# Kernel tuning notes

Measured on AMD Instinct MI355X. Metric: run time of the kernel, lower is better.

The kernel has to match this reference:

```python
import jax, jax.numpy as jnp
import numpy as np
import math

B, S, F, H, C = 64, 64, 4096, 1024, 31


def setup_inputs() -> dict:
    key = jax.random.key(0)
    ks = jax.random.split(key, 10)
    inp = {
        "x": jax.random.normal(ks[0], (B, S, F), dtype=jnp.float32),
        "h0": jax.random.normal(ks[1], (B, H), dtype=jnp.float32),
        "Wxe": jax.random.normal(ks[2], (F, H), dtype=jnp.float32) / math.sqrt(F),
        "bxe": jnp.zeros((H,), jnp.float32),
        "Wep": jax.random.normal(ks[3], (H, C), dtype=jnp.float32) / math.sqrt(H),
        "bep": jnp.zeros((C,), jnp.float32),
        "Whr": jax.random.normal(ks[4], (H, H), dtype=jnp.float32) / math.sqrt(H),
        "bhr": jnp.zeros((H,), jnp.float32),
        "Wx0r": jax.random.normal(ks[5], (H, H), dtype=jnp.float32) / math.sqrt(H),
        "bx0r": jnp.zeros((H,), jnp.float32),
        "Wxtz": jax.random.normal(ks[6], (H, H), dtype=jnp.float32) / math.sqrt(H),
        "bxtz": jnp.zeros((H,), jnp.float32),
        "Wx0z": jax.random.normal(ks[7], (H, H), dtype=jnp.float32) / math.sqrt(H),
        "bx0z": jnp.zeros((H,), jnp.float32),
        "Wxth1": jax.random.normal(ks[8], (H, H), dtype=jnp.float32) / math.sqrt(H),
        "bxth1": jnp.zeros((H,), jnp.float32),
        "Wh1h1": jax.random.normal(ks[9], (H, H), dtype=jnp.float32) / math.sqrt(H),
        "bh1h1": jnp.zeros((H,), jnp.float32),
    }
    return inp


def reference(x, h0, Wxe, bxe, Wep, bep, Whr, bhr, Wx0r, bx0r,
              Wxtz, bxtz, Wx0z, bx0z, Wxth1, bxth1, Wh1h1, bh1h1):
    # x: (B, S, F); h0: (B, H)
    steps = x.shape[1]
    x0 = x[:, -1]                                            # current information

    # Input-dependent projections are independent of the recurrence -> batch them.
    xtes = jax.nn.relu(jnp.einsum('bsf,fh->bsh', x, Wxe) + bxe)   # (B,S,H)
    x0e = jax.nn.relu(x0 @ Wxe + bxe)                             # (B,H), constant over steps
    ptes = jnp.einsum('bsh,hc->bsc', xtes, Wep) + bep             # (B,S,C)
    p0e = x0e @ Wep + bep                                         # (B,C)

    x0r = x0e @ Wx0r + bx0r                                       # (B,H) step-invariant
    x0z = x0e @ Wx0z + bx0z
    xtz_all = jnp.einsum('bsh,hg->bsg', xtes, Wxtz) + bxtz        # (B,S,H)
    xth1_all = jnp.einsum('bsh,hg->bsg', xtes, Wxth1) + bxth1     # (B,S,H)

    def step(h, inputs):
        xtz, xth1 = inputs                                        # (B,H) each
        rt = jax.nn.sigmoid(h @ Whr + bhr + x0r)
        zt = jax.nn.sigmoid(xtz + x0z)
        h1_t_1 = h @ Wh1h1 + bh1h1
        ht1 = jnp.tanh(xth1 + rt * h1_t_1)
        ht = (1.0 - zt) * ht1 + zt * h
        return ht, ht

    # scan over time: move step axis to front
    xs = (jnp.swapaxes(xtz_all, 0, 1), jnp.swapaxes(xth1_all, 0, 1))  # (S,B,H)
    _, hts_t = jax.lax.scan(step, h0, xs)
    hts = jnp.swapaxes(hts_t, 0, 1)                               # (B,S,H)

    p0es = jnp.broadcast_to(p0e[:, None, :], (p0e.shape[0], steps, p0e.shape[1]))
    x0es = jnp.broadcast_to(x0e[:, None, :], (x0e.shape[0], steps, x0e.shape[1]))
    return (hts, ptes, p0es, x0es * 1.0, xtes) if False else (hts, ptes, p0es, xtes, x0es)
```

## Files before the change

### kernel.cpp

```cpp
#include <hip/hip_runtime.h>
#include <stdint.h>


using bf16 = __bf16;
typedef __attribute__((ext_vector_type(8))) __bf16 bf16x8;
typedef __attribute__((ext_vector_type(4))) float f32x4;

#define B_DIM 64
#define S_DIM 64
#define F_DIM 4096
#define H_DIM 1024
#define C_DIM 31

__global__ void cast_tag_kernel(const float* __restrict__ x, bf16* __restrict__ xbf,
                                const float* __restrict__ h0, unsigned* __restrict__ hT0) {
  int bx = blockIdx.x;
  if (bx < 8192) {
    int i = bx * 256 + threadIdx.x;
    const float4* p = (const float4*)x + (size_t)i * 2;
    float4 a = p[0], b = p[1];
    bf16x8 v;
    v[0] = (bf16)a.x; v[1] = (bf16)a.y; v[2] = (bf16)a.z; v[3] = (bf16)a.w;
    v[4] = (bf16)b.x; v[5] = (bf16)b.y; v[6] = (bf16)b.z; v[7] = (bf16)b.w;
    ((bf16x8*)xbf)[i] = v;
  } else {
    int i = (bx - 8192) * 256 + threadIdx.x;
    union { bf16 b; unsigned short u; } cv;
    cv.b = (bf16)h0[i];
    __hip_atomic_store(hT0 + i, ((unsigned)cv.u << 16), __ATOMIC_RELAXED,
                       __HIP_MEMORY_SCOPE_AGENT);
  }
}

__device__ __forceinline__ void tr64(const float* __restrict__ in, bf16* __restrict__ out,
                                     int R, int C, int tR, int tC) {
  __shared__ float t[64][65];
  int tx = threadIdx.x & 63, ty = threadIdx.x >> 6;
#pragma unroll
  for (int i = 0; i < 16; ++i) {
    int r = tR + i * 4 + ty, c = tC + tx;
    t[i * 4 + ty][tx] = (r < R && c < C) ? in[(size_t)r * C + c] : 0.f;
  }
  __syncthreads();
#pragma unroll
  for (int i = 0; i < 16; ++i) {
    int c = tC + i * 4 + ty, r = tR + tx;
    if (c < C && r < R) out[(size_t)c * R + r] = (bf16)t[tx][i * 4 + ty];
  }
}

__global__ void transpose_all(const float* __restrict__ Wxe, bf16* __restrict__ WxeT,
                              const float* __restrict__ a0, const float* __restrict__ a1,
                              const float* __restrict__ a2, const float* __restrict__ a3,
                              const float* __restrict__ a4, const float* __restrict__ a5,
                              bf16* __restrict__ o0, bf16* __restrict__ o1,
                              bf16* __restrict__ o2,
                              const float* __restrict__ Wep, bf16* __restrict__ WepT) {
  int id = blockIdx.x;
  if (id < 1024) {
    tr64(Wxe, WxeT, 4096, 1024, (id & 63) * 64, (id >> 6) * 64);
  } else if (id < 2560) {
    int q = id - 1024, z = q >> 8, t = q & 255;
    const float* in = z == 0 ? a0 : z == 1 ? a1 : z == 2 ? a2 : z == 3 ? a3 : z == 4 ? a4 : a5;
    bf16* out = (z < 2 ? o0 : z < 4 ? o1 : o2) + (size_t)(z & 1) * 1048576;
    tr64(in, out, 1024, 1024, (t & 15) * 64, (t >> 4) * 64);
  } else {
    tr64(Wep, WepT, 1024, 31, (id - 2560) * 64, 0);
  }
}

__global__ void bcast_x0es(const float* __restrict__ xtesO, float* __restrict__ x0es) {
  int b = blockIdx.x >> 4, c = blockIdx.x & 15;
  float4 v = ((const float4*)(xtesO + ((size_t)b * 64 + 63) * 1024))[threadIdx.x];
  float4* dst = (float4*)(x0es + (size_t)b * 65536 + (size_t)c * 4096) + threadIdx.x;
#pragma unroll
  for (int i = 0; i < 4; ++i) dst[i * 256] = v;
}

template <int MODE>
__launch_bounds__(256, 2)
__global__ void gemm_bt(const bf16* __restrict__ A, const bf16* __restrict__ B,
                        int M, int N, int K, int lda,
                        const float* __restrict__ bias0,
                        const float* __restrict__ bias1,
                        const float* __restrict__ bias2,
                        const float* __restrict__ x0rz,
                        float* __restrict__ outA,
                        float* __restrict__ outB,
                        float* __restrict__ outC,
                        float* __restrict__ outD,
                        bf16* __restrict__ outBf) {
  __shared__ bf16 ldsA[128 * 64];
  __shared__ bf16 ldsB[128 * 64];
  const int tid = threadIdx.x;
  const int lane = tid & 63;
  const int wave = tid >> 6;
  const int quad = lane >> 4;
  const int l15 = lane & 15;
  const int wm = wave & 1, wn = wave >> 1;
  const int m0 = blockIdx.x * 128, n0 = blockIdx.y * 128;
  const int kPer = K / gridDim.z;
  const int k0 = blockIdx.z * kPer;

  f32x4 acc[4][4] = {};

  for (int kc = k0; kc < k0 + kPer; kc += 64) {
#pragma unroll
    for (int i = 0; i < 4; ++i) {
      int qb = i * 256 + wave * 64;
      int q = qb + lane;
      int r = q >> 3, cs = q & 7;
      int c = cs ^ (r & 7);
      int gr = m0 + r; if (gr > M - 1) gr = M - 1;
      __builtin_amdgcn_global_load_lds(
          (const __attribute__((address_space(1))) unsigned int*)(A + (size_t)gr * lda + kc + c * 8),
          (__attribute__((address_space(3))) unsigned int*)(ldsA + (size_t)qb * 8),
          16, 0, 0);
      __builtin_amdgcn_global_load_lds(
          (const __attribute__((address_space(1))) unsigned int*)(B + (size_t)(n0 + r) * K + kc + c * 8),
          (__attribute__((address_space(3))) unsigned int*)(ldsB + (size_t)qb * 8),
          16, 0, 0);
    }
    __syncthreads();
#pragma unroll
    for (int ks = 0; ks < 2; ++ks) {
      bf16x8 af[4], bfr[4];
      int ch = ks * 4 + quad;
#pragma unroll
      for (int t = 0; t < 4; ++t) {
        int ar = wm * 64 + t * 16 + l15;
        af[t] = *(const bf16x8*)(ldsA + ar * 64 + ((ch ^ (ar & 7)) * 8));
        int br = wn * 64 + t * 16 + l15;
        bfr[t] = *(const bf16x8*)(ldsB + br * 64 + ((ch ^ (br & 7)) * 8));
      }
#pragma unroll
      for (int mt = 0; mt < 4; ++mt)
#pragma unroll
        for (int nt = 0; nt < 4; ++nt)
          acc[mt][nt] = __builtin_amdgcn_mfma_f32_16x16x32_bf16(
              af[mt], bfr[nt], acc[mt][nt], 0, 0, 0);
    }
    __syncthreads();
  }

#pragma unroll
  for (int mt = 0; mt < 4; ++mt) {
#pragma unroll
    for (int nt = 0; nt < 4; ++nt) {
#pragma unroll
      for (int i = 0; i < 4; ++i) {
        int m = m0 + wm * 64 + mt * 16 + quad * 4 + i;
        int n = n0 + wn * 64 + nt * 16 + l15;
        if (m >= M) continue;
        float v = acc[mt][nt][i];
        if (MODE == 0) {
          v += bias0[n];
          v = fmaxf(v, 0.f);
          outA[(size_t)m * 1024 + n] = v;
          outBf[(size_t)m * 1024 + n] = (bf16)v;
        } else if (MODE == 1) {
          if (n < 1024) {
            float z = v + bias0[n] + x0rz[(size_t)(m >> 6) * 2048 + 1024 + n];
            outA[(size_t)m * 1024 + n] =
                __builtin_amdgcn_rcpf(1.f + __expf(-z));
          } else if (n < 2048) {
            outB[(size_t)m * 1024 + (n - 1024)] = v + bias1[n - 1024];
          } else if (n < 2048 + C_DIM) {
            float pv = v + bias2[n - 2048];
            outC[(size_t)m * C_DIM + (n - 2048)] = pv;
            if ((m & 63) == 63) {
              size_t base = (size_t)(m >> 6) * 64 * C_DIM + (n - 2048);
              for (int sp = 0; sp < 64; ++sp) outD[base + (size_t)sp * C_DIM] = pv;
            }
          }
        } else {
          if (k0 == 0) v += (n < 1024 ? bias0[n] : bias1[n - 1024]);
          atomicAdd(outA + (size_t)m * 2048 + n, v);
        }
      }
    }
  }
}

#define TAG_OK(v, w) \
  ((((unsigned)(v) & 0xFFFFu) == (w)) & (((unsigned)((v) >> 32) & 0xFFFFu) == (w)))

__launch_bounds__(256, 1)
__global__ void recur_kernel(const bf16* __restrict__ WrecT,
                             const float* __restrict__ bhr,
                             const float* __restrict__ bh1h1,
                             const float* __restrict__ x0rz,
                             const float* __restrict__ ztAll,
                             const float* __restrict__ xth1All,
                             const float* __restrict__ h0,
                             unsigned* hT0,
                             unsigned* hT1,
                             float* __restrict__ hts) {
  __shared__ bf16 ldsA[2][16 * 1024];
  const int tid = threadIdx.x;
  const int lane = tid & 63, wave = tid >> 6;
  const int quad = lane >> 4, l15 = lane & 15;
  const int j = blockIdx.x >> 2;
  const int g = blockIdx.x & 3;
  const int col = j * 64 + wave * 16 + l15;

  bf16x8 wr[32], wh[32];
#pragma unroll
  for (int kb = 0; kb < 32; ++kb) {
    wr[kb] = *(const bf16x8*)(WrecT + (size_t)col * 1024 + kb * 32 + quad * 8);
    wh[kb] = *(const bf16x8*)(WrecT + (size_t)(1024 + col) * 1024 + kb * 32 + quad * 8);
  }
  float hb_ = bh1h1[col];
  float rb[4], hloc[4];
#pragma unroll
  for (int i = 0; i < 4; ++i) {
    int b = g * 16 + quad * 4 + i;
    rb[i] = bhr[col] + x0rz[(size_t)b * 2048 + col];
    hloc[i] = h0[(size_t)b * 1024 + col];
  }

  const int off0 = ((quad ^ (l15 & 7)) * 16);
  const int off1 = (((4 + quad) ^ (l15 & 7)) * 16);

  for (int s = 0; s < 64; ++s) {
    const unsigned want = (unsigned)s;
    const unsigned long long* __restrict__ src =
        (const unsigned long long*)(((s & 1) ? hT1 : hT0) + (size_t)g * 16384) + tid * 2;

    unsigned long long qa[16], qb[16];
#pragma unroll
    for (int r = 0; r < 16; ++r) {
      qa[r] = __hip_atomic_load(src + (size_t)r * 512, __ATOMIC_RELAXED,
                                __HIP_MEMORY_SCOPE_AGENT);
      qb[r] = __hip_atomic_load(src + (size_t)r * 512 + 1, __ATOMIC_RELAXED,
                                __HIP_MEMORY_SCOPE_AGENT);
    }
    float zt[4], xh[4];
#pragma unroll
    for (int i = 0; i < 4; ++i) {
      size_t mrow = ((size_t)(g * 16 + quad * 4 + i) * 64 + s) * 1024 + col;
      zt[i] = ztAll[mrow];
      xh[i] = xth1All[mrow];
    }
    for (int it = 0; ; ++it) {
      unsigned miss = 0;
#pragma unroll
      for (int r = 0; r < 16; ++r)
        if (!(TAG_OK(qa[r], want) & TAG_OK(qb[r], want))) miss |= 1u << r;
      if (!miss || it > (1 << 17)) break;
#pragma unroll
      for (int r = 0; r < 16; ++r) {
        qa[r] = __hip_atomic_load(src + (size_t)r * 512, __ATOMIC_RELAXED,
                                  __HIP_MEMORY_SCOPE_AGENT);
        qb[r] = __hip_atomic_load(src + (size_t)r * 512 + 1, __ATOMIC_RELAXED,
                                  __HIP_MEMORY_SCOPE_AGENT);
      }
    }
    bf16* dstL = ldsA[s & 1];
#pragma unroll
    for (int r = 0; r < 16; ++r) {
      unsigned d0 = (unsigned)qa[r], d1 = (unsigned)(qa[r] >> 32);
      unsigned d2 = (unsigned)qb[r], d3 = (unsigned)(qb[r] >> 32);
      unsigned long long pk =
          ((unsigned long long)((d2 >> 16) | (d3 & 0xFFFF0000u)) << 32) |
          ((d0 >> 16) | (d1 & 0xFFFF0000u));
      int cc = ((tid >> 1) & 0x78) | (((tid >> 1) ^ r) & 7);
      *(unsigned long long*)((char*)dstL + r * 2048 + cc * 16 + (tid & 1) * 8) = pk;
    }
    __syncthreads();

    f32x4 racc0 = {0.f, 0.f, 0.f, 0.f}, racc1 = {0.f, 0.f, 0.f, 0.f};
    f32x4 hacc0 = {0.f, 0.f, 0.f, 0.f}, hacc1 = {0.f, 0.f, 0.f, 0.f};
    const char* baseL = (const char*)dstL + l15 * 2048;
#pragma unroll
    for (int kb = 0; kb < 32; kb += 2) {
      bf16x8 af0 = *(const bf16x8*)(baseL + (kb >> 1) * 128 + off0);
      bf16x8 af1 = *(const bf16x8*)(baseL + (kb >> 1) * 128 + off1);
      racc0 = __builtin_amdgcn_mfma_f32_16x16x32_bf16(af0, wr[kb], racc0, 0, 0, 0);
      hacc0 = __builtin_amdgcn_mfma_f32_16x16x32_bf16(af0, wh[kb], hacc0, 0, 0, 0);
      racc1 = __builtin_amdgcn_mfma_f32_16x16x32_bf16(af1, wr[kb + 1], racc1, 0, 0, 0);
      hacc1 = __builtin_amdgcn_mfma_f32_16x16x32_bf16(af1, wh[kb + 1], hacc1, 0, 0, 0);
    }

    unsigned* dst = (s & 1) ? hT0 : hT1;
    float hn[4];
#pragma unroll
    for (int i = 0; i < 4; ++i) {
      float ra = racc0[i] + racc1[i];
      float ha = hacc0[i] + hacc1[i];
      float rt = __builtin_amdgcn_rcpf(1.f + __expf(-(ra + rb[i])));
      float e2 = __expf(2.f * (xh[i] + rt * (ha + hb_)));
      float th = 1.f - 2.f * __builtin_amdgcn_rcpf(e2 + 1.f);
      hn[i] = (1.f - zt[i]) * th + zt[i] * hloc[i];
      hloc[i] = hn[i];
    }
    if (s < 63) {
#pragma unroll
      for (int i = 0; i < 4; ++i) {
        int b = g * 16 + quad * 4 + i;
        union { bf16 b16; unsigned short u; } cv;
        cv.b16 = (bf16)hn[i];
        __hip_atomic_store(dst + (size_t)b * 1024 + col,
                           ((unsigned)cv.u << 16) | (unsigned)(s + 1),
                           __ATOMIC_RELAXED, __HIP_MEMORY_SCOPE_AGENT);
      }
    }
#pragma unroll
    for (int i = 0; i < 4; ++i) {
      size_t mrow = ((size_t)(g * 16 + quad * 4 + i) * 64 + s) * 1024 + col;
      hts[mrow] = hn[i];
    }
  }
}

extern "C" void kernel_launch(void* const* d_in, const int* in_sizes, int n_in,
                              void* d_out, int out_size, void* d_ws, size_t ws_size,
                              hipStream_t stream) {
  const float* x     = (const float*)d_in[0];
  const float* h0    = (const float*)d_in[1];
  const float* Wxe   = (const float*)d_in[2];
  const float* bxe   = (const float*)d_in[3];
  const float* Wep   = (const float*)d_in[4];
  const float* bep   = (const float*)d_in[5];
  const float* Whr   = (const float*)d_in[6];
  const float* bhr   = (const float*)d_in[7];
  const float* Wx0r  = (const float*)d_in[8];
  const float* bx0r  = (const float*)d_in[9];
  const float* Wxtz  = (const float*)d_in[10];
  const float* bxtz  = (const float*)d_in[11];
  const float* Wx0z  = (const float*)d_in[12];
  const float* bx0z  = (const float*)d_in[13];
  const float* Wxth1 = (const float*)d_in[14];
  const float* bxth1 = (const float*)d_in[15];
  const float* Wh1h1 = (const float*)d_in[16];
  const float* bh1h1 = (const float*)d_in[17];

  float* out   = (float*)d_out;
  float* hts   = out;
  float* ptes  = out + 4194304;
  float* p0es  = out + 4321280;
  float* xtesO = out + 4448256;
  float* x0es  = out + 8642560;

  char* ws = (char*)d_ws;
  size_t off = 0;
  auto alloc = [&](size_t bytes) -> char* {
    char* p = ws + off;
    off += (bytes + 255) & ~(size_t)255;
    return p;
  };
  bf16*  xbf     = (bf16*)alloc(33554432);
  float* ztAll   = (float*)xbf;
  float* xth1All = (float*)((char*)xbf + 16777216);
  bf16*  WxeT    = (bf16*)alloc(8388608);
  bf16*  W2T     = (bf16*)alloc((size_t)2176 * 1024 * 2);
  bf16*  WrecT   = (bf16*)alloc(4194304);
  bf16*  Wx0T    = (bf16*)alloc(4194304);
  bf16*  xtesBf  = (bf16*)alloc(8388608);
  float* x0rz    = (float*)alloc(524288);
  unsigned* hT0  = (unsigned*)alloc(262144);
  unsigned* hT1  = (unsigned*)alloc(262144);

  hipMemsetAsync(W2T, 0, (size_t)2176 * 1024 * 2, stream);
  hipMemsetAsync(x0rz, 0, 524288, stream);

  dim3 tb(256);
  cast_tag_kernel<<<8448, tb, 0, stream>>>(x, xbf, h0, hT0);
  transpose_all<<<2576, tb, 0, stream>>>(Wxe, WxeT,
                                         Whr, Wh1h1, Wxtz, Wxth1, Wx0r, Wx0z,
                                         WrecT, W2T, Wx0T,
                                         Wep, W2T + 2048 * 1024);

  gemm_bt<0><<<dim3(32, 8), tb, 0, stream>>>(xbf, WxeT, 4096, 1024, 4096, 4096,
                                             bxe, nullptr, nullptr, nullptr,
                                             xtesO, nullptr, nullptr, nullptr, xtesBf);
  bcast_x0es<<<1024, tb, 0, stream>>>(xtesO, x0es);
  gemm_bt<2><<<dim3(1, 16, 4), tb, 0, stream>>>(xtesBf + 63 * 1024, Wx0T, 64, 2048, 1024, 65536,
                                                bx0r, bx0z, nullptr, nullptr,
                                                x0rz, nullptr, nullptr, nullptr, nullptr);
  gemm_bt<1><<<dim3(32, 17), tb, 0, stream>>>(xtesBf, W2T, 4096, 2176, 1024, 1024,
                                              bxtz, bxth1, bep, x0rz,
                                              ztAll, xth1All, ptes, p0es, nullptr);

  recur_kernel<<<64, tb, 0, stream>>>(WrecT, bhr, bh1h1, x0rz, ztAll, xth1All,
                                      h0, hT0, hT1, hts);
}
```

Before: 634.8 us.

## Split recurrence into 8 batch groups and add per-wave step flags for sync

The recurrent kernel now runs on 128 blocks, each handling 8 batch rows instead of 16. Only half the MFMA rows are used, and half of each wave's lanes sit idle in the elementwise part. Cross-block synchronisation moves from polling every tagged h value to polling a compact array of per-wave step flags. The h data is prefetched with sc0 loads before the flag spin, and the tag check is kept as a fallback. The goal is to shorten the serial per-step latency by spreading the step over more CUs and polling less data, at the cost of wasted MFMA work and a more complex memory-ordering protocol.

```diff
diff --git a/kernel.cpp b/kernel.cpp
--- a/kernel.cpp
+++ b/kernel.cpp
@@ -185,6 +185,16 @@
 #define TAG_OK(v, w) \
   ((((unsigned)(v) & 0xFFFFu) == (w)) & (((unsigned)((v) >> 32) & 0xFFFFu) == (w)))
 
+__device__ __forceinline__ unsigned long long sc0_load_u64(const unsigned long long* p) {
+  unsigned long long v;
+  asm volatile("global_load_dwordx2 %0, %1, off sc0" : "=v"(v) : "v"(p));
+  return v;
+}
+__device__ __forceinline__ void wait_vm0() {
+  asm volatile("s_waitcnt vmcnt(0)" ::: "memory");
+  __builtin_amdgcn_sched_barrier(0);
+}
+
 __launch_bounds__(256, 1)
 __global__ void recur_kernel(const bf16* __restrict__ WrecT,
                              const float* __restrict__ bhr,
@@ -195,13 +205,14 @@
                              const float* __restrict__ h0,
                              unsigned* hT0,
                              unsigned* hT1,
+                             unsigned* flags,
                              float* __restrict__ hts) {
-  __shared__ bf16 ldsA[2][16 * 1024];
+  __shared__ bf16 ldsA[2][8 * 1024];
   const int tid = threadIdx.x;
   const int lane = tid & 63, wave = tid >> 6;
   const int quad = lane >> 4, l15 = lane & 15;
-  const int j = blockIdx.x >> 2;
-  const int g = blockIdx.x & 3;
+  const int j = blockIdx.x >> 3;
+  const int g = blockIdx.x & 7;
   const int col = j * 64 + wave * 16 + l15;
 
   bf16x8 wr[32], wh[32];
@@ -211,54 +222,99 @@
     wh[kb] = *(const bf16x8*)(WrecT + (size_t)(1024 + col) * 1024 + kb * 32 + quad * 8);
   }
   float hb_ = bh1h1[col];
-  float rb[4], hloc[4];
-#pragma unroll
-  for (int i = 0; i < 4; ++i) {
-    int b = g * 16 + quad * 4 + i;
-    rb[i] = bhr[col] + x0rz[(size_t)b * 2048 + col];
-    hloc[i] = h0[(size_t)b * 1024 + col];
+  float rb[4] = {}, hloc[4] = {};
+  if (quad < 2) {
+#pragma unroll
+    for (int i = 0; i < 4; ++i) {
+      int b = g * 8 + quad * 4 + i;
+      rb[i] = bhr[col] + x0rz[(size_t)b * 2048 + col];
+      hloc[i] = h0[(size_t)b * 1024 + col];
+    }
   }
 
   const int off0 = ((quad ^ (l15 & 7)) * 16);
   const int off1 = (((4 + quad) ^ (l15 & 7)) * 16);
+
+  unsigned* fl = flags + g * 64;
+  const int myflag = j * 4 + wave;
 
   for (int s = 0; s < 64; ++s) {
     const unsigned want = (unsigned)s;
     const unsigned long long* __restrict__ src =
-        (const unsigned long long*)(((s & 1) ? hT1 : hT0) + (size_t)g * 16384) + tid * 2;
-
-    unsigned long long qa[16], qb[16];
-#pragma unroll
-    for (int r = 0; r < 16; ++r) {
-      qa[r] = __hip_atomic_load(src + (size_t)r * 512, __ATOMIC_RELAXED,
-                                __HIP_MEMORY_SCOPE_AGENT);
-      qb[r] = __hip_atomic_load(src + (size_t)r * 512 + 1, __ATOMIC_RELAXED,
-                                __HIP_MEMORY_SCOPE_AGENT);
-    }
-    float zt[4], xh[4];
-#pragma unroll
-    for (int i = 0; i < 4; ++i) {
-      size_t mrow = ((size_t)(g * 16 + quad * 4 + i) * 64 + s) * 1024 + col;
-      zt[i] = ztAll[mrow];
-      xh[i] = xth1All[mrow];
-    }
-    for (int it = 0; ; ++it) {
-      unsigned miss = 0;
-#pragma unroll
-      for (int r = 0; r < 16; ++r)
-        if (!(TAG_OK(qa[r], want) & TAG_OK(qb[r], want))) miss |= 1u << r;
-      if (!miss || it > (1 << 17)) break;
-#pragma unroll
-      for (int r = 0; r < 16; ++r) {
+        (const unsigned long long*)(((s & 1) ? hT1 : hT0) + (size_t)g * 8192) + tid * 2;
+
+    float zt[4] = {}, xh[4] = {};
+    if (quad < 2) {
+#pragma unroll
+      for (int i = 0; i < 4; ++i) {
+        size_t mrow = ((size_t)(g * 8 + quad * 4 + i) * 64 + s) * 1024 + col;
+        zt[i] = ztAll[mrow];
+        xh[i] = xth1All[mrow];
+      }
+    }
+
+    unsigned long long qa[8], qb[8];
+    if (s == 0) {
+#pragma unroll
+      for (int r = 0; r < 8; ++r) {
         qa[r] = __hip_atomic_load(src + (size_t)r * 512, __ATOMIC_RELAXED,
                                   __HIP_MEMORY_SCOPE_AGENT);
         qb[r] = __hip_atomic_load(src + (size_t)r * 512 + 1, __ATOMIC_RELAXED,
                                   __HIP_MEMORY_SCOPE_AGENT);
       }
-    }
+    } else {
+      bool have = false;
+      if (s < 63) {
+#pragma unroll
+        for (int r = 0; r < 8; ++r) {
+          qa[r] = sc0_load_u64(src + (size_t)r * 512);
+          qb[r] = sc0_load_u64(src + (size_t)r * 512 + 1);
+        }
+        wait_vm0();
+        have = true;
+      }
+      for (int round = 0; round < (1 << 18); ++round) {
+        unsigned f = __hip_atomic_load(fl + lane, __ATOMIC_RELAXED,
+                                       __HIP_MEMORY_SCOPE_AGENT);
+        if (__all((int)(f >= want))) break;
+      }
+      if (!have) {
+#pragma unroll
+        for (int r = 0; r < 8; ++r) {
+          qa[r] = sc0_load_u64(src + (size_t)r * 512);
+          qb[r] = sc0_load_u64(src + (size_t)r * 512 + 1);
+        }
+        wait_vm0();
+      }
+    }
+
+    for (int it = 0;; ++it) {
+      unsigned miss = 0;
+#pragma unroll
+      for (int r = 0; r < 8; ++r)
+        if (!(TAG_OK(qa[r], want) & TAG_OK(qb[r], want))) miss |= 1u << r;
+      if (!miss || it > (1 << 17)) break;
+      if (it & 1) {
+#pragma unroll
+        for (int r = 0; r < 8; ++r) {
+          qa[r] = __hip_atomic_load(src + (size_t)r * 512, __ATOMIC_RELAXED,
+                                    __HIP_MEMORY_SCOPE_AGENT);
+          qb[r] = __hip_atomic_load(src + (size_t)r * 512 + 1, __ATOMIC_RELAXED,
+                                    __HIP_MEMORY_SCOPE_AGENT);
+        }
+      } else {
+#pragma unroll
+        for (int r = 0; r < 8; ++r) {
+          qa[r] = sc0_load_u64(src + (size_t)r * 512);
+          qb[r] = sc0_load_u64(src + (size_t)r * 512 + 1);
+        }
+        wait_vm0();
+      }
+    }
+
     bf16* dstL = ldsA[s & 1];
 #pragma unroll
-    for (int r = 0; r < 16; ++r) {
+    for (int r = 0; r < 8; ++r) {
       unsigned d0 = (unsigned)qa[r], d1 = (unsigned)(qa[r] >> 32);
       unsigned d2 = (unsigned)qb[r], d3 = (unsigned)(qb[r] >> 32);
       unsigned long long pk =
@@ -271,7 +327,7 @@
 
     f32x4 racc0 = {0.f, 0.f, 0.f, 0.f}, racc1 = {0.f, 0.f, 0.f, 0.f};
     f32x4 hacc0 = {0.f, 0.f, 0.f, 0.f}, hacc1 = {0.f, 0.f, 0.f, 0.f};
-    const char* baseL = (const char*)dstL + l15 * 2048;
+    const char* baseL = (const char*)dstL + (l15 & 7) * 2048;
 #pragma unroll
     for (int kb = 0; kb < 32; kb += 2) {
       bf16x8 af0 = *(const bf16x8*)(baseL + (kb >> 1) * 128 + off0);
@@ -282,33 +338,43 @@
       hacc1 = __builtin_amdgcn_mfma_f32_16x16x32_bf16(af1, wh[kb + 1], hacc1, 0, 0, 0);
     }
 
+    float hn[4] = {};
     unsigned* dst = (s & 1) ? hT0 : hT1;
-    float hn[4];
-#pragma unroll
-    for (int i = 0; i < 4; ++i) {
-      float ra = racc0[i] + racc1[i];
-      float ha = hacc0[i] + hacc1[i];
-      float rt = __builtin_amdgcn_rcpf(1.f + __expf(-(ra + rb[i])));
-      float e2 = __expf(2.f * (xh[i] + rt * (ha + hb_)));
-      float th = 1.f - 2.f * __builtin_amdgcn_rcpf(e2 + 1.f);
-      hn[i] = (1.f - zt[i]) * th + zt[i] * hloc[i];
-      hloc[i] = hn[i];
-    }
-    if (s < 63) {
+    if (quad < 2) {
 #pragma unroll
       for (int i = 0; i < 4; ++i) {
-        int b = g * 16 + quad * 4 + i;
-        union { bf16 b16; unsigned short u; } cv;
-        cv.b16 = (bf16)hn[i];
-        __hip_atomic_store(dst + (size_t)b * 1024 + col,
-                           ((unsigned)cv.u << 16) | (unsigned)(s + 1),
-                           __ATOMIC_RELAXED, __HIP_MEMORY_SCOPE_AGENT);
-      }
-    }
-#pragma unroll
-    for (int i = 0; i < 4; ++i) {
-      size_t mrow = ((size_t)(g * 16 + quad * 4 + i) * 64 + s) * 1024 + col;
-      hts[mrow] = hn[i];
+        float ra = racc0[i] + racc1[i];
+        float ha = hacc0[i] + hacc1[i];
+        float rt = __builtin_amdgcn_rcpf(1.f + __expf(-(ra + rb[i])));
+        float e2 = __expf(2.f * (xh[i] + rt * (ha + hb_)));
+        float th = 1.f - 2.f * __builtin_amdgcn_rcpf(e2 + 1.f);
+        hn[i] = (1.f - zt[i]) * th + zt[i] * hloc[i];
+        hloc[i] = hn[i];
+      }
+      if (s < 63) {
+#pragma unroll
+        for (int i = 0; i < 4; ++i) {
+          int b = g * 8 + quad * 4 + i;
+          union { bf16 b16; unsigned short u; } cv;
+          cv.b16 = (bf16)hn[i];
+          unsigned pv = ((unsigned)cv.u << 16) | (unsigned)(s + 1);
+          unsigned* p = dst + (size_t)b * 1024 + col;
+          __hip_atomic_store(p, pv, __ATOMIC_RELAXED,
+                             __HIP_MEMORY_SCOPE_WORKGROUP);
+          __hip_atomic_store(p, pv, __ATOMIC_RELAXED,
+                             __HIP_MEMORY_SCOPE_AGENT);
+        }
+      }
+    }
+    if (lane == 0 && s < 63)
+      __hip_atomic_store(fl + myflag, want + 1, __ATOMIC_RELAXED,
+                         __HIP_MEMORY_SCOPE_AGENT);
+    if (quad < 2) {
+#pragma unroll
+      for (int i = 0; i < 4; ++i) {
+        size_t mrow = ((size_t)(g * 8 + quad * 4 + i) * 64 + s) * 1024 + col;
+        hts[mrow] = hn[i];
+      }
     }
   }
 }
@@ -360,9 +426,11 @@
   float* x0rz    = (float*)alloc(524288);
   unsigned* hT0  = (unsigned*)alloc(262144);
   unsigned* hT1  = (unsigned*)alloc(262144);
+  unsigned* flags = (unsigned*)alloc(2048);
 
   hipMemsetAsync(W2T, 0, (size_t)2176 * 1024 * 2, stream);
   hipMemsetAsync(x0rz, 0, 524288, stream);
+  hipMemsetAsync(flags, 0, 2048, stream);
 
   dim3 tb(256);
   cast_tag_kernel<<<8448, tb, 0, stream>>>(x, xbf, h0, hT0);
@@ -382,6 +450,6 @@
                                               bxtz, bxth1, bep, x0rz,
                                               ztAll, xth1All, ptes, p0es, nullptr);
 
-  recur_kernel<<<64, tb, 0, stream>>>(WrecT, bhr, bh1h1, x0rz, ztAll, xth1All,
-                                      h0, hT0, hT1, hts);
-}
+  recur_kernel<<<128, tb, 0, stream>>>(WrecT, bhr, bh1h1, x0rz, ztAll, xth1All,
+                                       h0, hT0, hT1, flags, hts);
+}
```

Result: slower. 791.5 us (+24.7%).
